# Optimization experiments

Hardware: AMD Instinct MI355X
Metric: run time of the kernel (lower is better)

## Reference

```python
import jax, jax.numpy as jnp
import numpy as np
from jax import lax

N_QUBITS = 8
DIM = 256  # 2**8 amplitudes
NUM_BLOCKS = 16
DEPTH = 1
ALPHA = 0.5
BATCH = 512

# Z-sign tables: qubit 0 is the most-significant bit of the flattened state index
_bits = (np.arange(DIM)[:, None] >> (N_QUBITS - 1 - np.arange(N_QUBITS))) & 1  # (256, 8)
_SIGNS = jnp.asarray(1.0 - 2.0 * _bits, dtype=jnp.float32)  # (256, 8)
_pairs = [(i, j) for i in range(N_QUBITS) for j in range(i + 1, N_QUBITS)]
_PAIR_SIGNS = jnp.stack([_SIGNS[:, i] * _SIGNS[:, j] for (i, j) in _pairs], axis=1)  # (256, 28)


def _apply_ry(state, c, s, q):
    # state: (N, 256) real (RY and CNOT keep the state real); gate on qubit q
    dl, dr = 2 ** q, 2 ** (N_QUBITS - 1 - q)
    st = state.reshape(-1, dl, 2, dr)
    s0, s1 = st[:, :, 0, :], st[:, :, 1, :]
    c_, s_ = c[:, None, None], s[:, None, None]
    n0 = c_ * s0 - s_ * s1
    n1 = s_ * s0 + c_ * s1
    return jnp.stack([n0, n1], axis=2).reshape(-1, DIM)


def _apply_cnot_chain(state, i):
    # CNOT control=i, target=i+1 (adjacent qubits)
    dl, dr = 2 ** i, 2 ** (N_QUBITS - 2 - i)
    st = state.reshape(-1, dl, 2, 2, dr)
    c0 = st[:, :, 0]                  # control=0: unchanged
    c1 = st[:, :, 1][:, :, ::-1]      # control=1: flip target bit
    return jnp.stack([c0, c1], axis=2).reshape(-1, DIM)


def _quantum_map(theta):
    # theta: (N, 8) -> (N, 36) [Z_i expectations (8) then Z_i Z_j for i<j (28)]
    half = 0.5 * theta
    c, s = jnp.cos(half), jnp.sin(half)
    state = jnp.zeros((theta.shape[0], DIM), dtype=theta.dtype).at[:, 0].set(1.0)
    for q in range(N_QUBITS):
        state = _apply_ry(state, c[:, q], s[:, q], q)
    for _ in range(DEPTH):
        for i in range(N_QUBITS - 1):
            state = _apply_cnot_chain(state, i)
    p = state * state  # probabilities (state is real)
    single = p @ _SIGNS          # (N, 8)
    two_body = p @ _PAIR_SIGNS   # (N, 28)
    return jnp.concatenate([single, two_body], axis=1)


def _bn(x, g, b, m, v):
    # inference-mode BatchNorm2d, eps=1e-5
    inv = g / jnp.sqrt(v + 1e-5)
    return x * inv[None, :, None, None] + (b - m * inv)[None, :, None, None]


def _conv(x, w, b):
    y = lax.conv_general_dilated(x, w, (1, 1), 'SAME',
                                 dimension_numbers=('NCHW', 'OIHW', 'NCHW'))
    return y + b[None, :, None, None]


def _maxpool2(x):
    return lax.reduce_window(x, -jnp.inf, lax.max, (1, 1, 2, 2), (1, 1, 2, 2), 'VALID')


def setup_inputs() -> dict:
    key = jax.random.key(0)
    ks = jax.random.split(key, 8)
    f32 = jnp.float32
    return {
        'x': jax.random.normal(ks[0], (BATCH, 3, 64, 64), dtype=f32),
        'conv1_w': jax.random.normal(ks[1], (16, 3, 3, 3), dtype=f32) * 0.1,
        'conv1_b': jnp.zeros((16,), f32),
        'bn1_g': jnp.ones((16,), f32), 'bn1_b': jnp.zeros((16,), f32),
        'bn1_m': jnp.zeros((16,), f32), 'bn1_v': jnp.ones((16,), f32),
        'conv2_w': jax.random.normal(ks[2], (32, 16, 3, 3), dtype=f32) * 0.08,
        'conv2_b': jnp.zeros((32,), f32),
        'bn2_g': jnp.ones((32,), f32), 'bn2_b': jnp.zeros((32,), f32),
        'bn2_m': jnp.zeros((32,), f32), 'bn2_v': jnp.ones((32,), f32),
        'conv3_w': jax.random.normal(ks[3], (64, 32, 3, 3), dtype=f32) * 0.06,
        'conv3_b': jnp.zeros((64,), f32),
        'bn3_g': jnp.ones((64,), f32), 'bn3_b': jnp.zeros((64,), f32),
        'bn3_m': jnp.zeros((64,), f32), 'bn3_v': jnp.ones((64,), f32),
        'proj_w': jax.random.normal(ks[4], (NUM_BLOCKS, 256, N_QUBITS), dtype=f32) * 0.06,
        'proj_b': jnp.zeros((NUM_BLOCKS, N_QUBITS), f32),
        'cls_w': jax.random.normal(ks[5], (10, NUM_BLOCKS * 36), dtype=f32) * 0.04,
        'cls_b': jnp.zeros((10,), f32),
    }


def reference(x, conv1_w, conv1_b, bn1_g, bn1_b, bn1_m, bn1_v,
              conv2_w, conv2_b, bn2_g, bn2_b, bn2_m, bn2_v,
              conv3_w, conv3_b, bn3_g, bn3_b, bn3_m, bn3_v,
              proj_w, proj_b, cls_w, cls_b):
    h = _maxpool2(jax.nn.relu(_bn(_conv(x, conv1_w, conv1_b), bn1_g, bn1_b, bn1_m, bn1_v)))
    h = _maxpool2(jax.nn.relu(_bn(_conv(h, conv2_w, conv2_b), bn2_g, bn2_b, bn2_m, bn2_v)))
    h = _maxpool2(jax.nn.relu(_bn(_conv(h, conv3_w, conv3_b), bn3_g, bn3_b, bn3_m, bn3_v)))
    B = h.shape[0]
    feats = h.reshape(B, NUM_BLOCKS, 256)  # 16 chunks of 256
    z = jnp.einsum('bkc,kcd->bkd', feats, proj_w) + proj_b[None]  # (B, 16, 8)
    theta = ALPHA * jnp.tanh(z)
    q_out = _quantum_map(theta.reshape(B * NUM_BLOCKS, N_QUBITS))  # (B*16, 36)
    combined = q_out.reshape(B, NUM_BLOCKS * 36)
    return combined @ cls_w.T + cls_b
```

## Files before the change

kernel.cpp:

```cpp
#include <hip/hip_runtime.h>
#include <hip/hip_bf16.h>
#include <math.h>

typedef __attribute__((ext_vector_type(8))) short short8;
typedef __attribute__((ext_vector_type(4))) float f32x4;

__device__ __forceinline__ unsigned short f2bf(float f) {
    union { float f; unsigned u; } x; x.f = f;
    unsigned r = x.u + 0x7FFF + ((x.u >> 16) & 1);
    return (unsigned short)(r >> 16);
}

__device__ __forceinline__ unsigned pk2bf(float a, float b) {
    union { __hip_bfloat162 h; unsigned u; } x;
    x.h = __float22bfloat162_rn(make_float2(a, b));
    return x.u;
}

__device__ __forceinline__ short8 mk8(uint2 a, uint2 b) {
    union { uint2 u[2]; short8 s; } x;
    x.u[0] = a; x.u[1] = b;
    return x.s;
}

__global__ void k_prep(const float* __restrict__ w2, const float* __restrict__ w3,
    const float* g2, const float* be2, const float* m2, const float* v2, const float* cb2,
    const float* g3, const float* be3, const float* m3, const float* v3, const float* cb3,
    const float* __restrict__ w1,
    const float* g1, const float* be1, const float* m1, const float* v1, const float* cb1,
    const float* __restrict__ pjw,
    unsigned short* __restrict__ wp2, unsigned short* __restrict__ wp3,
    unsigned short* __restrict__ wp1,
    float* __restrict__ cst2, float* __restrict__ cst3, float* __restrict__ cst1,
    float* __restrict__ pjwt)
{
    int tid = blockIdx.x * 256 + threadIdx.x;
    if (tid < 5120) {
        int j = tid & 7, lane = (tid >> 3) & 63, o = (tid >> 9) & 1, s = tid >> 10;
        int kl = ((lane >> 4) << 3) + j;
        int tp = s * 2 + (kl >> 4);
        int ic = kl & 15;
        int oc = o * 16 + (lane & 15);
        float val = (tp < 9) ? w2[(oc * 16 + ic) * 9 + tp] : 0.f;
        wp2[tid] = f2bf(val);
    } else if (tid < 23552) {
        int idx = tid - 5120;
        int j = idx & 7, lane = (idx >> 3) & 63, o = (idx >> 9) & 3, tap = idx >> 11;
        int ic = ((lane >> 4) << 3) + j;
        int oc = o * 16 + (lane & 15);
        wp3[idx] = f2bf(w3[(oc * 32 + ic) * 9 + tap]);
    } else if (tid < 23648) {
        int c = tid - 23552;
        if (c < 32) {
            float inv = g2[c] * rsqrtf(v2[c] + 1e-5f);
            cst2[c] = inv;
            cst2[32 + c] = (cb2[c] - m2[c]) * inv + be2[c];
        } else {
            int c3 = c - 32;
            float inv = g3[c3] * rsqrtf(v3[c3] + 1e-5f);
            cst3[c3] = inv;
            cst3[64 + c3] = (cb3[c3] - m3[c3]) * inv + be3[c3];
        }
    } else if (tid < 24672) {
        int idx = tid - 23648;
        int j = idx & 7, lane = (idx >> 3) & 63, s = (idx >> 9) & 1;
        int k = ((lane >> 4) << 3) + j;
        int oc = lane & 15;
        float val = 0.f;
        if (s == 0) {
            int tap = k >> 2, ic = k & 3;
            if (ic < 3) val = w1[(oc * 3 + ic) * 9 + tap];
        } else {
            if (k < 3) val = w1[(oc * 3 + k) * 9 + 8];
        }
        wp1[idx] = f2bf(val);
    } else if (tid < 24688) {
        int c = tid - 24672;
        float inv = g1[c] * rsqrtf(v1[c] + 1e-5f);
        cst1[c] = inv;
        cst1[16 + c] = (cb1[c] - m1[c]) * inv + be1[c];
    } else if (tid < 57456) {
        int idx = tid - 24688;
        int k = idx >> 11, d = (idx >> 8) & 7, c = idx & 255;
        pjwt[idx] = pjw[k * 2048 + c * 8 + d];
    }
}

__global__ __launch_bounds__(512, 4) void k_fused(
    const float* __restrict__ x,
    const unsigned short* __restrict__ wp1, const float* __restrict__ cst1,
    const unsigned short* __restrict__ wp2, const float* __restrict__ cst2,
    const unsigned short* __restrict__ wp3, const float* __restrict__ cst3,
    const float* __restrict__ pjwt, const float* __restrict__ pjb,
    const float* __restrict__ cw, const float* __restrict__ cbias,
    float* __restrict__ out)
{
    __shared__ __align__(16) unsigned char smem[57728];
    uint2* xse = (uint2*)smem;
    uint2* xso = xse + 34 * 33;
    unsigned short* h2tA = (unsigned short*)smem;
    unsigned short* h2tB = (unsigned short*)(smem + 10368);
    unsigned short* h1s  = (unsigned short*)(smem + 20736);
    float* feats = (float*)(smem + 20736);
    float* czs   = (float*)(smem + 20736 + 17408);
    float* partl = czs + 128;

    int b = blockIdx.x, t = threadIdx.x;
    int lane = t & 63, w = t >> 6, q = lane >> 4, xl = lane & 15;
    const float* img = x + (size_t)b * 12288;

    if (t < 264) {
        int arr = t & 3, idx = t >> 2;
        int row, slot;
        if (idx < 17)      { row = 0;        slot = idx; }
        else if (idx < 34) { row = 33;       slot = idx - 17; }
        else               { row = idx - 33; slot = (arr & 1) ? 0 : 16; }
        uint4 z = {0u, 0u, 0u, 0u};
        *(uint4*)(h1s + arr * 4624 + (row * 17 + slot) * 8) = z;
    }

    short8 A10 = *(const short8*)(wp1 + (lane << 3));
    short8 A11 = *(const short8*)(wp1 + ((64 + lane) << 3));
    int t0 = 2 * q, t1 = 2 * q + 1;
    int dy0 = t0 / 3 - 1, dx0 = t0 % 3 - 1;
    int dy1 = t1 / 3 - 1, dx1 = t1 % 3 - 1;
    float inv1[4], bs1[4];
    #pragma unroll
    for (int reg = 0; reg < 4; ++reg) {
        inv1[reg] = cst1[q * 4 + reg];
        bs1[reg]  = cst1[16 + q * 4 + reg];
    }
    #pragma unroll 1
    for (int h = 0; h < 2; ++h) {
        int y0 = h * 32 - 1;
        #pragma unroll 1
        for (int i = 0; i < 5; ++i) {
            int idx = t + i * 512;
            if (idx < 2244) {
                int y = idx / 66, xx = idx - y * 66;
                int c = xx - 1;
                int gy = y0 + y;
                float v0 = 0.f, v1 = 0.f, v2 = 0.f;
                if ((unsigned)gy < 64u && (unsigned)c < 64u) {
                    const float* pb = img + gy * 64 + c;
                    v0 = pb[0]; v1 = pb[4096]; v2 = pb[8192];
                }
                uint2 pk;
                pk.x = pk2bf(v0, v1);
                pk.y = pk2bf(v2, 0.f);
                int par = c & 1, slot = (c + par) >> 1;
                (par ? xso : xse)[y * 33 + slot] = pk;
            }
        }
        __syncthreads();
        unsigned* h1wbase = (unsigned*)(h1s + (q >> 1) * 2 * 4624);
        #pragma unroll 1
        for (int xTp = 0; xTp < 2; ++xTp) {
            int X = xTp * 16 + xl;
            float pv[4], vph[4];
            #pragma unroll
            for (int r = 0; r < 4; ++r) {
                int ly = w * 4 + r + 1;
                #pragma unroll
                for (int ph = 0; ph < 2; ++ph) {
                    int e0 = ph + dx0, e1 = ph + dx1, e2 = ph + 1;
                    const uint2* p0 = (e0 & 1) ? xso : xse;
                    const uint2* p1 = (e1 & 1) ? xso : xse;
                    const uint2* p2 = (e2 & 1) ? xso : xse;
                    uint2 ua = p0[(ly + dy0) * 33 + X + ((e0 + 1) >> 1)];
                    uint2 ub = p1[(ly + dy1) * 33 + X + ((e1 + 1) >> 1)];
                    uint2 uc = p2[(ly + 1) * 33 + X + ((e2 + 1) >> 1)];
                    f32x4 acc = (f32x4){0.f, 0.f, 0.f, 0.f};
                    acc = __builtin_amdgcn_mfma_f32_16x16x32_bf16(A10, mk8(ua, ub), acc, 0, 0, 0);
                    acc = __builtin_amdgcn_mfma_f32_16x16x32_bf16(A11, mk8(uc, uc), acc, 0, 0, 0);
                    #pragma unroll
                    for (int reg = 0; reg < 4; ++reg) {
                        float val = fmaxf(acc[reg] * inv1[reg] + bs1[reg], 0.f);
                        vph[reg] = ph ? fmaxf(vph[reg], val) : val;
                    }
                }
                if (r & 1) {
                    int py = h * 16 + w * 2 + (r >> 1);
                    int par = X & 1, slot = (X >> 1) + par;
                    unsigned* hp = h1wbase + par * 2312
                                   + ((py + 1) * 17 + slot) * 4 + (q & 1) * 2;
                    hp[0] = pk2bf(fmaxf(vph[0], pv[0]), fmaxf(vph[1], pv[1]));
                    hp[1] = pk2bf(fmaxf(vph[2], pv[2]), fmaxf(vph[3], pv[3]));
                } else {
                    #pragma unroll
                    for (int reg = 0; reg < 4; ++reg) pv[reg] = vph[reg];
                }
            }
        }
        __syncthreads();
    }

    if (t < 264) {
        int idx = t >> 1, half = t & 1;
        int y, xx;
        if (idx < 18)      { y = 0;        xx = idx; }
        else if (idx < 36) { y = 17;       xx = idx - 18; }
        else if (idx < 52) { y = idx - 35; xx = 0; }
        else if (idx < 68) { y = idx - 51; xx = 17; }
        else { y = -1; xx = 0; }
        if (y >= 0) {
            uint4 z = {0u, 0u, 0u, 0u};
            int pos = y * 18 + xx;
            *(uint4*)((half ? h2tB : h2tA) + pos * 16) = z;
            *(uint4*)((half ? h2tB : h2tA) + pos * 16 + 8) = z;
        }
    }

    {
        short8 A2[5][2];
        #pragma unroll
        for (int s = 0; s < 5; ++s)
            #pragma unroll
            for (int o = 0; o < 2; ++o)
                A2[s][o] = *(const short8*)(wp2 + (((s * 2 + o) * 64 + lane) << 3));
        int dyA[5], dxA[5];
        #pragma unroll
        for (int s = 0; s < 5; ++s) {
            int tp = s * 2 + (q >> 1); if (tp > 8) tp = 8;
            int d3 = tp / 3;
            dyA[s] = d3 - 1; dxA[s] = tp - d3 * 3 - 1;
        }
        const unsigned short* hb = h1s + (q & 1) * 2 * 4624;
        f32x4 acc[4][2][2];
        #pragma unroll
        for (int r = 0; r < 4; ++r)
            #pragma unroll
            for (int ph = 0; ph < 2; ++ph)
                #pragma unroll
                for (int o = 0; o < 2; ++o)
                    acc[r][ph][o] = (f32x4){0.f, 0.f, 0.f, 0.f};
        #pragma unroll
        for (int r = 0; r < 4; ++r) {
            int ry = w * 4 + r;
            #pragma unroll
            for (int ph = 0; ph < 2; ++ph) {
                #pragma unroll
                for (int s = 0; s < 5; ++s) {
                    int e = ph + dxA[s];
                    int row = ry + dyA[s] + 1;
                    int slot = xl + ((e + 1) >> 1);
                    const unsigned short* src = hb + (e & 1) * 4624;
                    short8 B = *(const short8*)(src + (row * 17 + slot) * 8);
                    acc[r][ph][0] = __builtin_amdgcn_mfma_f32_16x16x32_bf16(A2[s][0], B, acc[r][ph][0], 0, 0, 0);
                    acc[r][ph][1] = __builtin_amdgcn_mfma_f32_16x16x32_bf16(A2[s][1], B, acc[r][ph][1], 0, 0, 0);
                }
            }
        }
        #pragma unroll
        for (int oT = 0; oT < 2; ++oT)
            #pragma unroll
            for (int rp = 0; rp < 2; ++rp) {
                float vo[4];
                #pragma unroll
                for (int reg = 0; reg < 4; ++reg) {
                    int oc = oT * 16 + q * 4 + reg;
                    float iv = cst2[oc], bv = cst2[32 + oc];
                    float v00 = fmaxf(acc[rp * 2][0][oT][reg] * iv + bv, 0.f);
                    float v01 = fmaxf(acc[rp * 2][1][oT][reg] * iv + bv, 0.f);
                    float v10 = fmaxf(acc[rp * 2 + 1][0][oT][reg] * iv + bv, 0.f);
                    float v11 = fmaxf(acc[rp * 2 + 1][1][oT][reg] * iv + bv, 0.f);
                    vo[reg] = fmaxf(fmaxf(v00, v01), fmaxf(v10, v11));
                }
                int pos = (w * 2 + rp + 1) * 18 + (xl + 1);
                unsigned* hp = (unsigned*)(oT ? h2tB : h2tA) + pos * 8 + q * 2;
                hp[0] = pk2bf(vo[0], vo[1]);
                hp[1] = pk2bf(vo[2], vo[3]);
            }
    }
    __syncthreads();

    {
        int op = w & 1, rg = w >> 1;
        const unsigned short* h2r = (q < 2) ? h2tA : h2tB;
        short8 A3[9][2];
        #pragma unroll
        for (int tap = 0; tap < 9; ++tap)
            #pragma unroll
            for (int tt = 0; tt < 2; ++tt)
                A3[tap][tt] = *(const short8*)(wp3 + (((tap * 4 + op * 2 + tt) * 64 + lane) << 3));
        f32x4 acc[4][2];
        #pragma unroll
        for (int r = 0; r < 4; ++r) {
            acc[r][0] = (f32x4){0.f, 0.f, 0.f, 0.f};
            acc[r][1] = (f32x4){0.f, 0.f, 0.f, 0.f};
        }
        #pragma unroll
        for (int r = 0; r < 4; ++r) {
            int ry = rg * 4 + r + 1;
            #pragma unroll
            for (int tap = 0; tap < 9; ++tap) {
                int pos = (ry + tap / 3 - 1) * 18 + xl + (tap % 3);
                short8 B = *(const short8*)(h2r + pos * 16 + (q & 1) * 8);
                acc[r][0] = __builtin_amdgcn_mfma_f32_16x16x32_bf16(A3[tap][0], B, acc[r][0], 0, 0, 0);
                acc[r][1] = __builtin_amdgcn_mfma_f32_16x16x32_bf16(A3[tap][1], B, acc[r][1], 0, 0, 0);
            }
        }
        #pragma unroll
        for (int tt = 0; tt < 2; ++tt)
            #pragma unroll
            for (int reg = 0; reg < 4; ++reg) {
                int oc = (op * 2 + tt) * 16 + q * 4 + reg;
                float iv = cst3[oc], bv = cst3[64 + oc];
                #pragma unroll
                for (int rp = 0; rp < 2; ++rp) {
                    float v0 = fmaxf(acc[rp * 2][tt][reg] * iv + bv, 0.f);
                    float v1 = fmaxf(acc[rp * 2 + 1][tt][reg] * iv + bv, 0.f);
                    float vm = fmaxf(v0, v1);
                    float vv = fmaxf(vm, __shfl_xor(vm, 1, 64));
                    if (!(lane & 1))
                        feats[oc * 68 + (rg * 2 + rp) * 8 + (xl >> 1)] = vv;
                }
            }
    }
    __syncthreads();

    if (t < 128) {
        int k = t >> 3, d = t & 7;
        const float4* wrow = (const float4*)(pjwt + ((k * 8 + d) << 8));
        float zacc = 0.f;
        #pragma unroll 4
        for (int i = 0; i < 64; ++i) {
            int c4 = (i + k) & 63;
            float4 wv = wrow[c4];
            const float* fp = &feats[(k * 4 + (c4 >> 4)) * 68 + 4 * (c4 & 15)];
            float4 fv = *(const float4*)fp;
            zacc = fmaf(wv.x, fv.x, zacc);
            zacc = fmaf(wv.y, fv.y, zacc);
            zacc = fmaf(wv.z, fv.z, zacc);
            zacc = fmaf(wv.w, fv.w, zacc);
        }
        float z = zacc + pjb[k * 8 + d];
        czs[k * 8 + d] = cosf(0.5f * tanhf(z));
    }
    __syncthreads();
    if (t < 160) {
        int k = t / 10, c = t - (t / 10) * 10;
        float cz[8];
        #pragma unroll
        for (int i = 0; i < 8; ++i) cz[i] = czs[k * 8 + i];
        const float* cwp = cw + c * 576 + k * 36;
        float s = 0.f;
        float pp = 1.f;
        #pragma unroll
        for (int i = 0; i < 8; ++i) { pp *= cz[i]; s = fmaf(pp, cwp[i], s); }
        int cnt = 8;
        #pragma unroll
        for (int i = 0; i < 8; ++i) {
            float p2 = 1.f;
            #pragma unroll
            for (int j = i + 1; j < 8; ++j) { p2 *= cz[j]; s = fmaf(p2, cwp[cnt++], s); }
        }
        partl[k * 10 + c] = s;
    }
    __syncthreads();
    if (t < 10) {
        float s = cbias[t];
        #pragma unroll
        for (int k = 0; k < 16; ++k) s += partl[k * 10 + t];
        out[b * 10 + t] = s;
    }
}

extern "C" void kernel_launch(void* const* d_in, const int* in_sizes, int n_in,
                              void* d_out, int out_size, void* d_ws, size_t ws_size,
                              hipStream_t stream) {
    const float* x     = (const float*)d_in[0];
    const float* c1w   = (const float*)d_in[1];
    const float* c1b   = (const float*)d_in[2];
    const float* b1g   = (const float*)d_in[3];
    const float* b1b   = (const float*)d_in[4];
    const float* b1m   = (const float*)d_in[5];
    const float* b1v   = (const float*)d_in[6];
    const float* c2w   = (const float*)d_in[7];
    const float* c2b   = (const float*)d_in[8];
    const float* b2g   = (const float*)d_in[9];
    const float* b2b   = (const float*)d_in[10];
    const float* b2m   = (const float*)d_in[11];
    const float* b2v   = (const float*)d_in[12];
    const float* c3w   = (const float*)d_in[13];
    const float* c3b   = (const float*)d_in[14];
    const float* b3g   = (const float*)d_in[15];
    const float* b3b   = (const float*)d_in[16];
    const float* b3m   = (const float*)d_in[17];
    const float* b3v   = (const float*)d_in[18];
    const float* pjw   = (const float*)d_in[19];
    const float* pjb   = (const float*)d_in[20];
    const float* cw    = (const float*)d_in[21];
    const float* cbias = (const float*)d_in[22];
    float* outp = (float*)d_out;

    unsigned char* prep = (unsigned char*)d_ws;
    unsigned short* wp2 = (unsigned short*)prep;
    unsigned short* wp3 = (unsigned short*)(prep + 16384);
    unsigned short* wp1 = (unsigned short*)(prep + 16384 + 36864);
    float* cst2 = (float*)(prep + 16384 + 36864 + 2048);
    float* cst3 = cst2 + 64;
    float* cst1 = cst3 + 128;
    float* pjwt = (float*)(prep + 16384 + 36864 + 2048 + 1024);

    k_prep<<<225, 256, 0, stream>>>(c2w, c3w, b2g, b2b, b2m, b2v, c2b,
                                    b3g, b3b, b3m, b3v, c3b,
                                    c1w, b1g, b1b, b1m, b1v, c1b, pjw,
                                    wp2, wp3, wp1, cst2, cst3, cst1, pjwt);
    k_fused<<<512, 512, 0, stream>>>(x, wp1, cst1, wp2, cst2, wp3, cst3,
                                     pjwt, pjb, cw, cbias, outp);
}
```

Baseline: 136.9 us.

## Drop weight-prep kernel and pack bf16 weights inside the fused kernel

Removes the separate k_prep launch that repacked conv weights into bf16 MFMA fragments, folded BatchNorm constants and transposed the projection weights. The fused kernel now gathers and converts the raw fp32 weights itself, using strided global loads, and recomputes the BN scale and shift per block. The projection reduction is spread across all 512 threads with a partial-sum buffer and an extra barrier, replacing the 128-thread float4 loop. This saves one launch and its dependency, but every block now does redundant, uncoalesced weight loads and conversions.

```diff
diff --git a/kernel.cpp b/kernel.cpp
--- a/kernel.cpp
+++ b/kernel.cpp
@@ -23,75 +23,27 @@
     return x.s;
 }
 
-__global__ void k_prep(const float* __restrict__ w2, const float* __restrict__ w3,
-    const float* g2, const float* be2, const float* m2, const float* v2, const float* cb2,
-    const float* g3, const float* be3, const float* m3, const float* v3, const float* cb3,
-    const float* __restrict__ w1,
-    const float* g1, const float* be1, const float* m1, const float* v1, const float* cb1,
-    const float* __restrict__ pjw,
-    unsigned short* __restrict__ wp2, unsigned short* __restrict__ wp3,
-    unsigned short* __restrict__ wp1,
-    float* __restrict__ cst2, float* __restrict__ cst3, float* __restrict__ cst1,
-    float* __restrict__ pjwt)
-{
-    int tid = blockIdx.x * 256 + threadIdx.x;
-    if (tid < 5120) {
-        int j = tid & 7, lane = (tid >> 3) & 63, o = (tid >> 9) & 1, s = tid >> 10;
-        int kl = ((lane >> 4) << 3) + j;
-        int tp = s * 2 + (kl >> 4);
-        int ic = kl & 15;
-        int oc = o * 16 + (lane & 15);
-        float val = (tp < 9) ? w2[(oc * 16 + ic) * 9 + tp] : 0.f;
-        wp2[tid] = f2bf(val);
-    } else if (tid < 23552) {
-        int idx = tid - 5120;
-        int j = idx & 7, lane = (idx >> 3) & 63, o = (idx >> 9) & 3, tap = idx >> 11;
-        int ic = ((lane >> 4) << 3) + j;
-        int oc = o * 16 + (lane & 15);
-        wp3[idx] = f2bf(w3[(oc * 32 + ic) * 9 + tap]);
-    } else if (tid < 23648) {
-        int c = tid - 23552;
-        if (c < 32) {
-            float inv = g2[c] * rsqrtf(v2[c] + 1e-5f);
-            cst2[c] = inv;
-            cst2[32 + c] = (cb2[c] - m2[c]) * inv + be2[c];
-        } else {
-            int c3 = c - 32;
-            float inv = g3[c3] * rsqrtf(v3[c3] + 1e-5f);
-            cst3[c3] = inv;
-            cst3[64 + c3] = (cb3[c3] - m3[c3]) * inv + be3[c3];
-        }
-    } else if (tid < 24672) {
-        int idx = tid - 23648;
-        int j = idx & 7, lane = (idx >> 3) & 63, s = (idx >> 9) & 1;
-        int k = ((lane >> 4) << 3) + j;
-        int oc = lane & 15;
-        float val = 0.f;
-        if (s == 0) {
-            int tap = k >> 2, ic = k & 3;
-            if (ic < 3) val = w1[(oc * 3 + ic) * 9 + tap];
-        } else {
-            if (k < 3) val = w1[(oc * 3 + k) * 9 + 8];
-        }
-        wp1[idx] = f2bf(val);
-    } else if (tid < 24688) {
-        int c = tid - 24672;
-        float inv = g1[c] * rsqrtf(v1[c] + 1e-5f);
-        cst1[c] = inv;
-        cst1[16 + c] = (cb1[c] - m1[c]) * inv + be1[c];
-    } else if (tid < 57456) {
-        int idx = tid - 24688;
-        int k = idx >> 11, d = (idx >> 8) & 7, c = idx & 255;
-        pjwt[idx] = pjw[k * 2048 + c * 8 + d];
-    }
+__device__ __forceinline__ short8 pack8(const unsigned short* e) {
+    union { unsigned u[4]; short8 s; } x;
+    x.u[0] = (unsigned)e[0] | ((unsigned)e[1] << 16);
+    x.u[1] = (unsigned)e[2] | ((unsigned)e[3] << 16);
+    x.u[2] = (unsigned)e[4] | ((unsigned)e[5] << 16);
+    x.u[3] = (unsigned)e[6] | ((unsigned)e[7] << 16);
+    return x.s;
 }
 
 __global__ __launch_bounds__(512, 4) void k_fused(
     const float* __restrict__ x,
-    const unsigned short* __restrict__ wp1, const float* __restrict__ cst1,
-    const unsigned short* __restrict__ wp2, const float* __restrict__ cst2,
-    const unsigned short* __restrict__ wp3, const float* __restrict__ cst3,
-    const float* __restrict__ pjwt, const float* __restrict__ pjb,
+    const float* __restrict__ w1,
+    const float* __restrict__ g1, const float* __restrict__ be1,
+    const float* __restrict__ m1, const float* __restrict__ v1, const float* __restrict__ cb1,
+    const float* __restrict__ w2,
+    const float* __restrict__ g2, const float* __restrict__ be2,
+    const float* __restrict__ m2, const float* __restrict__ v2, const float* __restrict__ cb2,
+    const float* __restrict__ w3,
+    const float* __restrict__ g3, const float* __restrict__ be3,
+    const float* __restrict__ m3, const float* __restrict__ v3, const float* __restrict__ cb3,
+    const float* __restrict__ pjw, const float* __restrict__ pjb,
     const float* __restrict__ cw, const float* __restrict__ cbias,
     float* __restrict__ out)
 {
@@ -103,7 +55,8 @@
     unsigned short* h1s  = (unsigned short*)(smem + 20736);
     float* feats = (float*)(smem + 20736);
     float* czs   = (float*)(smem + 20736 + 17408);
-    float* partl = czs + 128;
+    float* zpart = czs + 128;
+    float* partl = zpart + 512;
 
     int b = blockIdx.x, t = threadIdx.x;
     int lane = t & 63, w = t >> 6, q = lane >> 4, xl = lane & 15;
@@ -119,17 +72,32 @@
         *(uint4*)(h1s + arr * 4624 + (row * 17 + slot) * 8) = z;
     }
 
-    short8 A10 = *(const short8*)(wp1 + (lane << 3));
-    short8 A11 = *(const short8*)(wp1 + ((64 + lane) << 3));
+    short8 A10, A11;
+    {
+        unsigned short e[8];
+        #pragma unroll
+        for (int j = 0; j < 8; ++j) {
+            int ic = j & 3, tap = q * 2 + (j >> 2);
+            e[j] = (ic < 3) ? f2bf(w1[(xl * 3 + ic) * 9 + tap]) : (unsigned short)0;
+        }
+        A10 = pack8(e);
+        #pragma unroll
+        for (int j = 0; j < 8; ++j)
+            e[j] = (q == 0 && j < 3) ? f2bf(w1[(xl * 3 + j) * 9 + 8]) : (unsigned short)0;
+        A11 = pack8(e);
+    }
     int t0 = 2 * q, t1 = 2 * q + 1;
     int dy0 = t0 / 3 - 1, dx0 = t0 % 3 - 1;
     int dy1 = t1 / 3 - 1, dx1 = t1 % 3 - 1;
     float inv1[4], bs1[4];
     #pragma unroll
     for (int reg = 0; reg < 4; ++reg) {
-        inv1[reg] = cst1[q * 4 + reg];
-        bs1[reg]  = cst1[16 + q * 4 + reg];
-    }
+        int oc = q * 4 + reg;
+        float inv = g1[oc] * rsqrtf(v1[oc] + 1e-5f);
+        inv1[reg] = inv;
+        bs1[reg]  = (cb1[oc] - m1[oc]) * inv + be1[oc];
+    }
+
     #pragma unroll 1
     for (int h = 0; h < 2; ++h) {
         int y0 = h * 32 - 1;
@@ -140,14 +108,14 @@
                 int y = idx / 66, xx = idx - y * 66;
                 int c = xx - 1;
                 int gy = y0 + y;
-                float v0 = 0.f, v1 = 0.f, v2 = 0.f;
+                float v0 = 0.f, v1v = 0.f, v2v = 0.f;
                 if ((unsigned)gy < 64u && (unsigned)c < 64u) {
                     const float* pb = img + gy * 64 + c;
-                    v0 = pb[0]; v1 = pb[4096]; v2 = pb[8192];
+                    v0 = pb[0]; v1v = pb[4096]; v2v = pb[8192];
                 }
                 uint2 pk;
-                pk.x = pk2bf(v0, v1);
-                pk.y = pk2bf(v2, 0.f);
+                pk.x = pk2bf(v0, v1v);
+                pk.y = pk2bf(v2v, 0.f);
                 int par = c & 1, slot = (c + par) >> 1;
                 (par ? xso : xse)[y * 33 + slot] = pk;
             }
@@ -213,15 +181,27 @@
 
     {
         short8 A2[5][2];
+        int tps = q >> 1, icb = (q & 1) * 8;
         #pragma unroll
         for (int s = 0; s < 5; ++s)
             #pragma unroll
-            for (int o = 0; o < 2; ++o)
-                A2[s][o] = *(const short8*)(wp2 + (((s * 2 + o) * 64 + lane) << 3));
+            for (int o = 0; o < 2; ++o) {
+                int tp = s * 2 + tps;
+                unsigned short e[8];
+                if (tp < 9) {
+                    const float* wsrc = w2 + (((o * 16 + xl) * 16 + icb) * 9) + tp;
+                    #pragma unroll
+                    for (int j = 0; j < 8; ++j) e[j] = f2bf(wsrc[j * 9]);
+                } else {
+                    #pragma unroll
+                    for (int j = 0; j < 8; ++j) e[j] = 0;
+                }
+                A2[s][o] = pack8(e);
+            }
         int dyA[5], dxA[5];
         #pragma unroll
         for (int s = 0; s < 5; ++s) {
-            int tp = s * 2 + (q >> 1); if (tp > 8) tp = 8;
+            int tp = s * 2 + tps; if (tp > 8) tp = 8;
             int d3 = tp / 3;
             dyA[s] = d3 - 1; dxA[s] = tp - d3 * 3 - 1;
         }
@@ -259,7 +239,8 @@
                 #pragma unroll
                 for (int reg = 0; reg < 4; ++reg) {
                     int oc = oT * 16 + q * 4 + reg;
-                    float iv = cst2[oc], bv = cst2[32 + oc];
+                    float iv = g2[oc] * rsqrtf(v2[oc] + 1e-5f);
+                    float bv = (cb2[oc] - m2[oc]) * iv + be2[oc];
                     float v00 = fmaxf(acc[rp * 2][0][oT][reg] * iv + bv, 0.f);
                     float v01 = fmaxf(acc[rp * 2][1][oT][reg] * iv + bv, 0.f);
                     float v10 = fmaxf(acc[rp * 2 + 1][0][oT][reg] * iv + bv, 0.f);
@@ -281,8 +262,13 @@
         #pragma unroll
         for (int tap = 0; tap < 9; ++tap)
             #pragma unroll
-            for (int tt = 0; tt < 2; ++tt)
-                A3[tap][tt] = *(const short8*)(wp3 + (((tap * 4 + op * 2 + tt) * 64 + lane) << 3));
+            for (int tt = 0; tt < 2; ++tt) {
+                const float* wsrc = w3 + ((((op * 2 + tt) * 16 + xl) * 32 + q * 8) * 9) + tap;
+                unsigned short e[8];
+                #pragma unroll
+                for (int j = 0; j < 8; ++j) e[j] = f2bf(wsrc[j * 9]);
+                A3[tap][tt] = pack8(e);
+            }
         f32x4 acc[4][2];
         #pragma unroll
         for (int r = 0; r < 4; ++r) {
@@ -305,7 +291,8 @@
             #pragma unroll
             for (int reg = 0; reg < 4; ++reg) {
                 int oc = (op * 2 + tt) * 16 + q * 4 + reg;
-                float iv = cst3[oc], bv = cst3[64 + oc];
+                float iv = g3[oc] * rsqrtf(v3[oc] + 1e-5f);
+                float bv = (cb3[oc] - m3[oc]) * iv + be3[oc];
                 #pragma unroll
                 for (int rp = 0; rp < 2; ++rp) {
                     float v0 = fmaxf(acc[rp * 2][tt][reg] * iv + bv, 0.f);
@@ -319,22 +306,24 @@
     }
     __syncthreads();
 
+    {
+        int g = t >> 2, p = t & 3;
+        int k = g >> 3, d = g & 7;
+        const float* wsrc = pjw + k * 2048 + (p * 64) * 8 + d;
+        const float* fsrc = &feats[(k * 4 + p) * 68];
+        float za = 0.f, zb = 0.f;
+        #pragma unroll 8
+        for (int pos = 0; pos < 64; pos += 2) {
+            za = fmaf(wsrc[pos * 8],     fsrc[pos],     za);
+            zb = fmaf(wsrc[pos * 8 + 8], fsrc[pos + 1], zb);
+        }
+        zpart[t] = za + zb;
+    }
+    __syncthreads();
     if (t < 128) {
         int k = t >> 3, d = t & 7;
-        const float4* wrow = (const float4*)(pjwt + ((k * 8 + d) << 8));
-        float zacc = 0.f;
-        #pragma unroll 4
-        for (int i = 0; i < 64; ++i) {
-            int c4 = (i + k) & 63;
-            float4 wv = wrow[c4];
-            const float* fp = &feats[(k * 4 + (c4 >> 4)) * 68 + 4 * (c4 & 15)];
-            float4 fv = *(const float4*)fp;
-            zacc = fmaf(wv.x, fv.x, zacc);
-            zacc = fmaf(wv.y, fv.y, zacc);
-            zacc = fmaf(wv.z, fv.z, zacc);
-            zacc = fmaf(wv.w, fv.w, zacc);
-        }
-        float z = zacc + pjb[k * 8 + d];
+        float z = (zpart[t * 4] + zpart[t * 4 + 1]) + (zpart[t * 4 + 2] + zpart[t * 4 + 3])
+                  + pjb[k * 8 + d];
         czs[k * 8 + d] = cosf(0.5f * tanhf(z));
     }
     __syncthreads();
@@ -394,19 +383,9 @@
     const float* cbias = (const float*)d_in[22];
     float* outp = (float*)d_out;
 
-    unsigned char* prep = (unsigned char*)d_ws;
-    unsigned short* wp2 = (unsigned short*)prep;
-    unsigned short* wp3 = (unsigned short*)(prep + 16384);
-    unsigned short* wp1 = (unsigned short*)(prep + 16384 + 36864);
-    float* cst2 = (float*)(prep + 16384 + 36864 + 2048);
-    float* cst3 = cst2 + 64;
-    float* cst1 = cst3 + 128;
-    float* pjwt = (float*)(prep + 16384 + 36864 + 2048 + 1024);
-
-    k_prep<<<225, 256, 0, stream>>>(c2w, c3w, b2g, b2b, b2m, b2v, c2b,
-                                    b3g, b3b, b3m, b3v, c3b,
-                                    c1w, b1g, b1b, b1m, b1v, c1b, pjw,
-                                    wp2, wp3, wp1, cst2, cst3, cst1, pjwt);
-    k_fused<<<512, 512, 0, stream>>>(x, wp1, cst1, wp2, cst2, wp3, cst3,
-                                     pjwt, pjb, cw, cbias, outp);
-}
+    k_fused<<<512, 512, 0, stream>>>(x,
+        c1w, b1g, b1b, b1m, b1v, c1b,
+        c2w, b2g, b2b, b2m, b2v, c2b,
+        c3w, b3g, b3b, b3m, b3v, c3b,
+        pjw, pjb, cw, cbias, outp);
+}
```

New measurement: 215.7 us. +57.5%, slower.
